# Performance work log

Measured on AMD Instinct MI355X. Metric: run time of the kernel, lower is better.

## Reference

```python
import jax, jax.numpy as jnp
import numpy as np

H = 1024      # embe_size / hidden size
L = 2         # layer_num
LBL = 5       # label_size
B, S = 64, 512


def setup_inputs() -> dict:
    key = jax.random.key(0)
    ks = jax.random.split(key, 7)
    sc = 1.0 / np.sqrt(H)
    inputs = jax.random.normal(ks[0], (B, S, H), dtype=jnp.float32)
    Wx = jax.random.uniform(ks[1], (L, H, 4 * H), minval=-sc, maxval=sc, dtype=jnp.float32)
    bx = jax.random.uniform(ks[2], (L, 4 * H), minval=-sc, maxval=sc, dtype=jnp.float32)
    Wh = jax.random.uniform(ks[3], (L, H, 4 * H), minval=-sc, maxval=sc, dtype=jnp.float32)
    bh = jax.random.uniform(ks[4], (L, 4 * H), minval=-sc, maxval=sc, dtype=jnp.float32)
    scp = 1.0 / np.sqrt(H)
    Wp = jax.random.uniform(ks[5], (H, LBL), minval=-scp, maxval=scp, dtype=jnp.float32)
    bp = jax.random.uniform(ks[6], (LBL,), minval=-scp, maxval=scp, dtype=jnp.float32)
    return {"inputs": inputs, "Wx": Wx, "bx": bx, "Wh": Wh, "bh": bh, "Wp": Wp, "bp": bp}


def _lstm_forward(inputs, Wx, bx, Wh, bh, Wp, bp):
    # inputs: [B,S,H] -> time-major [S,B,H]
    x = jnp.transpose(inputs, (1, 0, 2))
    n_layers = Wx.shape[0]
    bsz, hid = x.shape[1], Wx.shape[1]
    for l in range(n_layers):
        Wh_l, bh_l = Wh[l], bh[l]
        # precompute input->gate projection for all timesteps: [S,B,4H]
        xg = jnp.einsum('sbh,hg->sbg', x, Wx[l]) + bx[l]

        def step(carry, xg_t):
            h, c = carry
            feat = xg_t + h @ Wh_l + bh_l
            i, f, g, o = jnp.split(feat, 4, axis=-1)
            c = jax.nn.sigmoid(f) * c + jax.nn.sigmoid(i) * jnp.tanh(g)
            h = jnp.tanh(c) * jax.nn.sigmoid(o)
            return (h, c), h

        h0 = jnp.zeros((bsz, hid), dtype=x.dtype)
        _, x = jax.lax.scan(step, (h0, h0), xg)
        # dropout is identity at inference (eval mode)
    # max-pool over time (max_pool1d over full seq), then classify
    pooled = jnp.max(x, axis=0)  # [B,H]
    return pooled @ Wp + bp      # [B,label_size]


def reference(inputs, Wx, bx, Wh, bh, Wp, bp):
    return _lstm_forward(inputs, Wx, bx, Wh, bh, Wp, bp)
```

## Files before the change

### kernel.cpp

```cpp
#include <hip/hip_runtime.h>
#include <hip/hip_bf16.h>

typedef _Float16 half8 __attribute__((ext_vector_type(8)));
typedef _Float16 half4v __attribute__((ext_vector_type(4)));
typedef float f32x4 __attribute__((ext_vector_type(4)));

#define BB 64
#define SS 512
#define HH 1024
#define G4 4096
#define NSTEP 514
#define SLOT 65536

#define SB_ARR(g) ((g) * 32)
#define SB_GLB 256
#define SB_GO(g) (288 + (g) * 32)
#define FB_ARR(L, g) ((L) * 256 + (g) * 32)
#define FB_GLB(L) (512 + (L) * 32)
#define FB_GO(L, g) (576 + (L) * 256 + (g) * 32)

__device__ __forceinline__ float sigmf(float x) { return 1.0f / (1.0f + __expf(-x)); }
__device__ __forceinline__ float tanhfast(float x) { return 2.0f / (1.0f + __expf(-2.0f * x)) - 1.0f; }

__device__ __forceinline__ unsigned aload(const unsigned* p) {
  return __hip_atomic_load(p, __ATOMIC_RELAXED, __HIP_MEMORY_SCOPE_AGENT);
}
__device__ __forceinline__ void wait_ge(const unsigned* p, unsigned tgt) {
  while (aload(p) < tgt) __builtin_amdgcn_s_sleep(1);
}
__device__ __forceinline__ unsigned aadd(unsigned* p) {
  return __hip_atomic_fetch_add(p, 1u, __ATOMIC_RELAXED, __HIP_MEMORY_SCOPE_AGENT);
}
__device__ __forceinline__ void astore(unsigned* p, unsigned v) {
  __hip_atomic_store(p, v, __ATOMIC_RELAXED, __HIP_MEMORY_SCOPE_AGENT);
}

__global__ __launch_bounds__(256) void convert_x_kernel(const float* __restrict__ in,
                                                        _Float16* __restrict__ x16) {
  size_t idx = (size_t)blockIdx.x * 256 + threadIdx.x;
  int h4 = (int)(idx & 255);
  int s  = (int)((idx >> 8) & 511);
  int b  = (int)(idx >> 17);
  const float4* src = (const float4*)in;
  float4 v = src[((size_t)b * SS + s) * 256 + h4];
  half4v hv = { (_Float16)v.x, (_Float16)v.y, (_Float16)v.z, (_Float16)v.w };
  *(half4v*)(x16 + ((size_t)s * BB + b) * HH + (size_t)h4 * 4) = hv;
}

__global__ __launch_bounds__(256) void convert_w_kernel(const float* __restrict__ Wx,
                                                        const float* __restrict__ Wh,
                                                        _Float16* __restrict__ wT) {
  __shared__ float tile[32][33];
  int m = blockIdx.x >> 12;
  int t = blockIdx.x & 4095;
  int tn = t & 127, tk = t >> 7;
  int l = m & 1, which = m >> 1;
  const float* src = (which ? Wh : Wx) + (size_t)l * HH * G4;
  int tx = threadIdx.x & 31, ty = threadIdx.x >> 5;
#pragma unroll
  for (int p = 0; p < 4; ++p) {
    int k = tk * 32 + ty + 8 * p, n = tn * 32 + tx;
    tile[ty + 8 * p][tx] = src[(size_t)k * G4 + n];
  }
  __syncthreads();
  _Float16* dst = wT + (size_t)m * G4 * HH;
#pragma unroll
  for (int p = 0; p < 4; ++p) {
    int n = tn * 32 + ty + 8 * p, k = tk * 32 + tx;
    dst[(size_t)n * HH + k] = (_Float16)tile[tx][ty + 8 * p];
  }
}

template <bool TRAJ>
__global__ __launch_bounds__(512, 2) void lstm_persist(
    const _Float16* __restrict__ x16, const _Float16* __restrict__ wT,
    const float* __restrict__ bx, const float* __restrict__ bh,
    _Float16* __restrict__ h1buf, _Float16* __restrict__ h2buf,
    float* __restrict__ hmax, unsigned* __restrict__ bar) {
  __shared__ float part[8][32][72];
  __shared__ float red[64][37];

  const int bid = blockIdx.x;
  const int layer = bid >> 7;
  const int j = bid & 127;
  const int tid = threadIdx.x;
  const int w = tid >> 6, l = tid & 63;
  const int l15 = l & 15, lg = l >> 4;
  const int grp = bid & 7;

  const _Float16* wTe = wT + (size_t)layer * G4 * HH;
  const _Float16* wTr = wT + (size_t)(2 + layer) * G4 * HH;
  const int kbase = w * 128;
  half8 Be[8], Br[8];
#pragma unroll
  for (int kk = 0; kk < 4; ++kk)
#pragma unroll
    for (int c = 0; c < 2; ++c) {
      int nl = 16 * c + l15;
      size_t gcol = (size_t)((nl & 3) * HH + 8 * j + (nl >> 2));
      Be[kk * 2 + c] = *(const half8*)(wTe + gcol * HH + kbase + 32 * kk + 8 * lg);
      Br[kk * 2 + c] = *(const half8*)(wTr + gcol * HH + kbase + 32 * kk + 8 * lg);
    }

  const int erow = tid >> 2, m2 = tid & 3;
  const int hc0 = 8 * j + 2 * m2;
  float bs[8];
  float c0 = 0.f, c1 = 0.f, hm0 = -2.f, hm1 = -2.f;
  if (tid < 256) {
#pragma unroll
    for (int dm = 0; dm < 2; ++dm)
#pragma unroll
      for (int g = 0; g < 4; ++g)
        bs[4 * dm + g] = bx[layer * G4 + g * HH + hc0 + dm] + bh[layer * G4 + g * HH + hc0 + dm];
  }

  const int tmax = TRAJ ? (layer ? NSTEP : SS) : NSTEP;

#pragma unroll 1
  for (int t = 0; t < tmax; ++t) {
    const bool act = (layer == 0) ? (t < SS) : (t >= 2);
    f32x4 acc[8];
#pragma unroll
    for (int i = 0; i < 8; ++i) acc[i] = (f32x4){0.f, 0.f, 0.f, 0.f};

    if (act) {
      const _Float16* Ae;
      if (layer == 0) {
        Ae = x16 + (size_t)t * SLOT;
      } else if (TRAJ) {
        if (tid == 0) wait_ge(bar + FB_GO(0, grp), (unsigned)(t - 1));
        __syncthreads();
        Ae = h1buf + (size_t)(t - 1) * SLOT;
      } else {
        Ae = h1buf + (size_t)((t - 2) & 3) * SLOT;
      }
      const _Float16* aep = Ae + (size_t)l15 * HH + kbase + 8 * lg;
      half8 a[16];
#pragma unroll
      for (int rf = 0; rf < 4; ++rf)
#pragma unroll
        for (int kk = 0; kk < 4; ++kk)
          a[rf * 4 + kk] = *(const half8*)(aep + (size_t)(16 * rf) * HH + 32 * kk);
#pragma unroll
      for (int rf = 0; rf < 4; ++rf)
#pragma unroll
        for (int kk = 0; kk < 4; ++kk) {
          acc[rf * 2 + 0] = __builtin_amdgcn_mfma_f32_16x16x32_f16(a[rf * 4 + kk], Be[kk * 2 + 0], acc[rf * 2 + 0], 0, 0, 0);
          acc[rf * 2 + 1] = __builtin_amdgcn_mfma_f32_16x16x32_f16(a[rf * 4 + kk], Be[kk * 2 + 1], acc[rf * 2 + 1], 0, 0, 0);
        }
    }

    if (tid == 0) {
      if (TRAJ) {
        wait_ge(bar + FB_GO(layer, grp), (unsigned)t);
      } else {
        wait_ge(bar + SB_GO(grp), (unsigned)t);
        __builtin_amdgcn_fence(__ATOMIC_ACQUIRE, "agent");
      }
    }
    __syncthreads();

    if (act) {
      const _Float16* Ah;
      if (layer == 0)
        Ah = TRAJ ? h1buf + (size_t)t * SLOT
                  : h1buf + (size_t)((t - 1) & 3) * SLOT;
      else
        Ah = TRAJ ? h2buf + (size_t)(t - 2) * SLOT
                  : h2buf + (size_t)((t - 1) & 1) * SLOT;
      const _Float16* ahp = Ah + (size_t)l15 * HH + kbase + 8 * lg;
      half8 a[16];
#pragma unroll
      for (int rf = 0; rf < 4; ++rf)
#pragma unroll
        for (int kk = 0; kk < 4; ++kk)
          a[rf * 4 + kk] = *(const half8*)(ahp + (size_t)(16 * rf) * HH + 32 * kk);
#pragma unroll
      for (int rf = 0; rf < 4; ++rf)
#pragma unroll
        for (int kk = 0; kk < 4; ++kk) {
          acc[rf * 2 + 0] = __builtin_amdgcn_mfma_f32_16x16x32_f16(a[rf * 4 + kk], Br[kk * 2 + 0], acc[rf * 2 + 0], 0, 0, 0);
          acc[rf * 2 + 1] = __builtin_amdgcn_mfma_f32_16x16x32_f16(a[rf * 4 + kk], Br[kk * 2 + 1], acc[rf * 2 + 1], 0, 0, 0);
        }

#pragma unroll
      for (int rf = 0; rf < 4; ++rf)
#pragma unroll
        for (int c = 0; c < 2; ++c)
          *(f32x4*)&part[w][16 * c + l15][16 * rf + 4 * lg] = acc[rf * 2 + c];
      __syncthreads();

      {
        int col = tid >> 4, rq = tid & 15;
        f32x4 s = {0.f, 0.f, 0.f, 0.f};
#pragma unroll
        for (int ww = 0; ww < 8; ++ww)
          s += *(const f32x4*)&part[ww][col][4 * rq];
        red[4 * rq + 0][col] = s[0];
        red[4 * rq + 1][col] = s[1];
        red[4 * rq + 2][col] = s[2];
        red[4 * rq + 3][col] = s[3];
      }
      __syncthreads();

      if (tid < 256) {
        float v[8];
#pragma unroll
        for (int q = 0; q < 8; ++q) v[q] = red[erow][8 * m2 + q] + bs[q];
        float i0 = sigmf(v[0]), f0 = sigmf(v[1]), g0 = tanhfast(v[2]), o0 = sigmf(v[3]);
        float i1 = sigmf(v[4]), f1 = sigmf(v[5]), g1 = tanhfast(v[6]), o1 = sigmf(v[7]);
        c0 = f0 * c0 + i0 * g0;
        c1 = f1 * c1 + i1 * g1;
        float h0 = tanhfast(c0) * o0;
        float h1 = tanhfast(c1) * o1;
        if (layer == 1) { hm0 = fmaxf(hm0, h0); hm1 = fmaxf(hm1, h1); }
        _Float16* hout;
        if (layer == 0)
          hout = TRAJ ? h1buf + (size_t)(t + 1) * SLOT : h1buf + (size_t)(t & 3) * SLOT;
        else
          hout = TRAJ ? h2buf + (size_t)(t - 1) * SLOT : h2buf + (size_t)(t & 1) * SLOT;
        unsigned pk = ((unsigned)__builtin_bit_cast(unsigned short, (_Float16)h1) << 16) |
                      (unsigned)__builtin_bit_cast(unsigned short, (_Float16)h0);
        astore((unsigned*)hout + ((erow * HH + hc0) >> 1), pk);
      }
    }

    __syncthreads();
    if (tid == 0) {
      if (TRAJ) {
        unsigned prev = aadd(bar + FB_ARR(layer, grp));
        if (prev == 16u * (unsigned)(t + 1) - 1u) {
          unsigned p2 = aadd(bar + FB_GLB(layer));
          if (p2 == 8u * (unsigned)(t + 1) - 1u) {
#pragma unroll
            for (int gg = 0; gg < 8; ++gg)
              astore(bar + FB_GO(layer, gg), (unsigned)(t + 1));
          }
        }
      } else {
        unsigned prev = aadd(bar + SB_ARR(grp));
        if (prev == 32u * (unsigned)(t + 1) - 1u) {
          unsigned p2 = aadd(bar + SB_GLB);
          if (p2 == 8u * (unsigned)(t + 1) - 1u) {
#pragma unroll
            for (int gg = 0; gg < 8; ++gg)
              astore(bar + SB_GO(gg), (unsigned)(t + 1));
          }
        }
      }
    }
  }

  if (layer == 1 && tid < 256) {
    hmax[erow * HH + hc0]     = hm0;
    hmax[erow * HH + hc0 + 1] = hm1;
  }
}

__global__ __launch_bounds__(320) void classify_kernel(const float* __restrict__ hmax,
                                                       const float* __restrict__ Wp,
                                                       const float* __restrict__ bp,
                                                       float* __restrict__ out) {
  int tid = threadIdx.x;
  int b = tid / 5, jj = tid % 5;
  float s = bp[jj];
  const float* hp = hmax + (size_t)b * HH;
  for (int h = 0; h < HH; ++h) s = fmaf(hp[h], Wp[h * 5 + jj], s);
  out[tid] = s;
}

extern "C" void kernel_launch(void* const* d_in, const int* in_sizes, int n_in,
                              void* d_out, int out_size, void* d_ws, size_t ws_size,
                              hipStream_t stream) {
  const float* inputs = (const float*)d_in[0];
  const float* Wx = (const float*)d_in[1];
  const float* bx = (const float*)d_in[2];
  const float* Wh = (const float*)d_in[3];
  const float* bh = (const float*)d_in[4];
  const float* Wp = (const float*)d_in[5];
  const float* bp = (const float*)d_in[6];
  float* out = (float*)d_out;

  char* ws = (char*)d_ws;
  _Float16* x16 = (_Float16*)(ws + 0);
  _Float16* wT  = (_Float16*)(ws + 67108864);

  const size_t TRAJ_BYTES = (size_t)513 * 131072;
  const size_t NEED_FAST = 100663296ull + 2 * TRAJ_BYTES + 262144 + 8192;
  bool fast = ws_size >= NEED_FAST;

  convert_x_kernel<<<32768, 256, 0, stream>>>(inputs, x16);
  convert_w_kernel<<<16384, 256, 0, stream>>>(Wx, Wh, wT);

  if (fast) {
    _Float16* h1traj = (_Float16*)(ws + 100663296);
    _Float16* h2traj = (_Float16*)(ws + 100663296 + TRAJ_BYTES);
    float* hmax = (float*)(ws + 100663296 + 2 * TRAJ_BYTES);
    unsigned* bar = (unsigned*)(ws + 100663296 + 2 * TRAJ_BYTES + 262144);
    hipMemsetAsync(h1traj, 0, 131072, stream);
    hipMemsetAsync(h2traj, 0, 131072, stream);
    hipMemsetAsync(bar, 0, 8192, stream);
    lstm_persist<true><<<256, 512, 0, stream>>>(x16, wT, bx, bh, h1traj, h2traj, hmax, bar);
    classify_kernel<<<1, 320, 0, stream>>>(hmax, Wp, bp, out);
  } else {
    _Float16* h1buf = (_Float16*)(ws + 100663296);
    _Float16* h2buf = (_Float16*)(ws + 101187584);
    float* hmax = (float*)(ws + 101449728);
    unsigned* bar = (unsigned*)(ws + 101711872);
    hipMemsetAsync(h1buf, 0, 524288, stream);
    hipMemsetAsync(h2buf, 0, 262144, stream);
    hipMemsetAsync(bar, 0, 8192, stream);
    lstm_persist<false><<<256, 512, 0, stream>>>(x16, wT, bx, bh, h1buf, h2buf, hmax, bar);
    classify_kernel<<<1, 320, 0, stream>>>(hmax, Wp, bp, out);
  }
}
```

Measured before the change: 4.822 ms.

## Fuse both LSTM layers into one 128-block persistent kernel with a single barrier

Replaces the 256-block persistent kernel (one layer per block, with separate per-layer barriers) with 128 blocks. Each block computes the same hidden column slice for both layers: waves 0-3 handle layer 0 and waves 4-7 handle layer 1, each over a K range of 256. One grid-wide barrier per step serves both layers, which removes the cross-layer wait and halves the number of barrier participants. In exchange, each wave holds twice as many weight fragments in registers and does twice the MFMA work per step, and only 128 CUs are used. The spin-wait sleep interval is also raised.

```diff
diff --git a/kernel.cpp b/kernel.cpp
--- a/kernel.cpp
+++ b/kernel.cpp
@@ -15,9 +15,9 @@
 #define SB_ARR(g) ((g) * 32)
 #define SB_GLB 256
 #define SB_GO(g) (288 + (g) * 32)
-#define FB_ARR(L, g) ((L) * 256 + (g) * 32)
-#define FB_GLB(L) (512 + (L) * 32)
-#define FB_GO(L, g) (576 + (L) * 256 + (g) * 32)
+#define FU_ARR(g) ((g) * 32)
+#define FU_GLB 256
+#define FU_GO(g) (288 + (g) * 32)
 
 __device__ __forceinline__ float sigmf(float x) { return 1.0f / (1.0f + __expf(-x)); }
 __device__ __forceinline__ float tanhfast(float x) { return 2.0f / (1.0f + __expf(-2.0f * x)) - 1.0f; }
@@ -26,7 +26,7 @@
   return __hip_atomic_load(p, __ATOMIC_RELAXED, __HIP_MEMORY_SCOPE_AGENT);
 }
 __device__ __forceinline__ void wait_ge(const unsigned* p, unsigned tgt) {
-  while (aload(p) < tgt) __builtin_amdgcn_s_sleep(1);
+  while (aload(p) < tgt) __builtin_amdgcn_s_sleep(4);
 }
 __device__ __forceinline__ unsigned aadd(unsigned* p) {
   return __hip_atomic_fetch_add(p, 1u, __ATOMIC_RELAXED, __HIP_MEMORY_SCOPE_AGENT);
@@ -71,8 +71,154 @@
   }
 }
 
-template <bool TRAJ>
-__global__ __launch_bounds__(512, 2) void lstm_persist(
+__global__ __launch_bounds__(512, 2) void lstm_fused(
+    const _Float16* __restrict__ x16, const _Float16* __restrict__ wT,
+    const float* __restrict__ bx, const float* __restrict__ bh,
+    _Float16* __restrict__ h1buf, _Float16* __restrict__ h2buf,
+    float* __restrict__ hmax, unsigned* __restrict__ bar) {
+  __shared__ float part[8][32][72];
+  __shared__ float red[64][68];
+
+  const int bid = blockIdx.x;
+  const int j = bid;
+  const int tid = threadIdx.x;
+  const int w = tid >> 6, l = tid & 63;
+  const int l15 = l & 15, lg = l >> 4;
+  const int grp = bid & 7;
+  const int wlayer = w >> 2;
+  const int kbase = (w & 3) * 256;
+
+  const _Float16* wTe = wT + (size_t)wlayer * G4 * HH;
+  const _Float16* wTr = wT + (size_t)(2 + wlayer) * G4 * HH;
+  half8 Be[16], Br[16];
+#pragma unroll
+  for (int kk = 0; kk < 8; ++kk)
+#pragma unroll
+    for (int c = 0; c < 2; ++c) {
+      int nl = 16 * c + l15;
+      size_t gcol = (size_t)((nl & 3) * HH + 8 * j + (nl >> 2));
+      Be[kk * 2 + c] = *(const half8*)(wTe + gcol * HH + kbase + 32 * kk + 8 * lg);
+      Br[kk * 2 + c] = *(const half8*)(wTr + gcol * HH + kbase + 32 * kk + 8 * lg);
+    }
+
+  const int elayer = tid >> 8;
+  const int erow = (tid & 255) >> 2, m2 = tid & 3;
+  const int hc0 = 8 * j + 2 * m2;
+  float bs[8];
+  float c0 = 0.f, c1 = 0.f, hm0 = -2.f, hm1 = -2.f;
+#pragma unroll
+  for (int dm = 0; dm < 2; ++dm)
+#pragma unroll
+    for (int g = 0; g < 4; ++g)
+      bs[4 * dm + g] = bx[elayer * G4 + g * HH + hc0 + dm] + bh[elayer * G4 + g * HH + hc0 + dm];
+
+#pragma unroll 1
+  for (int t = 0; t < NSTEP; ++t) {
+    const bool wact = wlayer ? (t >= 2) : (t < SS);
+    f32x4 acc[8];
+#pragma unroll
+    for (int i = 0; i < 8; ++i) acc[i] = (f32x4){0.f, 0.f, 0.f, 0.f};
+
+    if (wact) {
+      const _Float16* Ae = (wlayer == 0) ? x16 + (size_t)t * SLOT
+                                         : h1buf + (size_t)(t - 1) * SLOT;
+      const _Float16* aep = Ae + (size_t)l15 * HH + kbase + 8 * lg;
+#pragma unroll
+      for (int rf = 0; rf < 4; ++rf) {
+        half8 av[8];
+#pragma unroll
+        for (int kk = 0; kk < 8; ++kk)
+          av[kk] = *(const half8*)(aep + (size_t)(16 * rf) * HH + 32 * kk);
+#pragma unroll
+        for (int kk = 0; kk < 8; ++kk) {
+          acc[rf * 2 + 0] = __builtin_amdgcn_mfma_f32_16x16x32_f16(av[kk], Be[kk * 2 + 0], acc[rf * 2 + 0], 0, 0, 0);
+          acc[rf * 2 + 1] = __builtin_amdgcn_mfma_f32_16x16x32_f16(av[kk], Be[kk * 2 + 1], acc[rf * 2 + 1], 0, 0, 0);
+        }
+      }
+    }
+
+    if (tid == 0) wait_ge(bar + FU_GO(grp), (unsigned)t);
+    __syncthreads();
+
+    if (wact) {
+      const _Float16* Ah = (wlayer == 0) ? h1buf + (size_t)t * SLOT
+                                         : h2buf + (size_t)(t - 2) * SLOT;
+      const _Float16* ahp = Ah + (size_t)l15 * HH + kbase + 8 * lg;
+#pragma unroll
+      for (int rf = 0; rf < 4; ++rf) {
+        half8 av[8];
+#pragma unroll
+        for (int kk = 0; kk < 8; ++kk)
+          av[kk] = *(const half8*)(ahp + (size_t)(16 * rf) * HH + 32 * kk);
+#pragma unroll
+        for (int kk = 0; kk < 8; ++kk) {
+          acc[rf * 2 + 0] = __builtin_amdgcn_mfma_f32_16x16x32_f16(av[kk], Br[kk * 2 + 0], acc[rf * 2 + 0], 0, 0, 0);
+          acc[rf * 2 + 1] = __builtin_amdgcn_mfma_f32_16x16x32_f16(av[kk], Br[kk * 2 + 1], acc[rf * 2 + 1], 0, 0, 0);
+        }
+      }
+#pragma unroll
+      for (int rf = 0; rf < 4; ++rf)
+#pragma unroll
+        for (int c = 0; c < 2; ++c)
+          *(f32x4*)&part[w][16 * c + l15][16 * rf + 4 * lg] = acc[rf * 2 + c];
+    }
+    __syncthreads();
+
+#pragma unroll
+    for (int sidx = 0; sidx < 2; ++sidx) {
+      int s = tid + 512 * sidx;
+      int L = s >> 9, col = (s >> 4) & 31, rq = s & 15;
+      f32x4 sum = {0.f, 0.f, 0.f, 0.f};
+#pragma unroll
+      for (int ww = 0; ww < 4; ++ww)
+        sum += *(const f32x4*)&part[4 * L + ww][col][4 * rq];
+      red[4 * rq + 0][col + 32 * L] = sum[0];
+      red[4 * rq + 1][col + 32 * L] = sum[1];
+      red[4 * rq + 2][col + 32 * L] = sum[2];
+      red[4 * rq + 3][col + 32 * L] = sum[3];
+    }
+    __syncthreads();
+
+    const bool eact = elayer ? (t >= 2) : (t < SS);
+    if (eact) {
+      float v[8];
+#pragma unroll
+      for (int q = 0; q < 8; ++q) v[q] = red[erow][32 * elayer + 8 * m2 + q] + bs[q];
+      float i0 = sigmf(v[0]), f0 = sigmf(v[1]), g0 = tanhfast(v[2]), o0 = sigmf(v[3]);
+      float i1 = sigmf(v[4]), f1 = sigmf(v[5]), g1 = tanhfast(v[6]), o1 = sigmf(v[7]);
+      c0 = f0 * c0 + i0 * g0;
+      c1 = f1 * c1 + i1 * g1;
+      float h0 = tanhfast(c0) * o0;
+      float h1 = tanhfast(c1) * o1;
+      if (elayer == 1) { hm0 = fmaxf(hm0, h0); hm1 = fmaxf(hm1, h1); }
+      _Float16* hout = (elayer == 0) ? h1buf + (size_t)(t + 1) * SLOT
+                                     : h2buf + (size_t)(t - 1) * SLOT;
+      unsigned pk = ((unsigned)__builtin_bit_cast(unsigned short, (_Float16)h1) << 16) |
+                    (unsigned)__builtin_bit_cast(unsigned short, (_Float16)h0);
+      astore((unsigned*)hout + ((erow * HH + hc0) >> 1), pk);
+    }
+
+    __syncthreads();
+    if (tid == 0) {
+      unsigned prev = aadd(bar + FU_ARR(grp));
+      if (prev == 16u * (unsigned)(t + 1) - 1u) {
+        unsigned p2 = aadd(bar + FU_GLB);
+        if (p2 == 8u * (unsigned)(t + 1) - 1u) {
+#pragma unroll
+          for (int gg = 0; gg < 8; ++gg)
+            astore(bar + FU_GO(gg), (unsigned)(t + 1));
+        }
+      }
+    }
+  }
+
+  if (tid >= 256) {
+    hmax[erow * HH + hc0]     = hm0;
+    hmax[erow * HH + hc0 + 1] = hm1;
+  }
+}
+
+__global__ __launch_bounds__(512, 2) void lstm_safe(
     const _Float16* __restrict__ x16, const _Float16* __restrict__ wT,
     const float* __restrict__ bx, const float* __restrict__ bh,
     _Float16* __restrict__ h1buf, _Float16* __restrict__ h2buf,
@@ -114,26 +260,16 @@
         bs[4 * dm + g] = bx[layer * G4 + g * HH + hc0 + dm] + bh[layer * G4 + g * HH + hc0 + dm];
   }
 
-  const int tmax = TRAJ ? (layer ? NSTEP : SS) : NSTEP;
-
 #pragma unroll 1
-  for (int t = 0; t < tmax; ++t) {
+  for (int t = 0; t < NSTEP; ++t) {
     const bool act = (layer == 0) ? (t < SS) : (t >= 2);
     f32x4 acc[8];
 #pragma unroll
     for (int i = 0; i < 8; ++i) acc[i] = (f32x4){0.f, 0.f, 0.f, 0.f};
 
     if (act) {
-      const _Float16* Ae;
-      if (layer == 0) {
-        Ae = x16 + (size_t)t * SLOT;
-      } else if (TRAJ) {
-        if (tid == 0) wait_ge(bar + FB_GO(0, grp), (unsigned)(t - 1));
-        __syncthreads();
-        Ae = h1buf + (size_t)(t - 1) * SLOT;
-      } else {
-        Ae = h1buf + (size_t)((t - 2) & 3) * SLOT;
-      }
+      const _Float16* Ae = (layer == 0) ? x16 + (size_t)t * SLOT
+                                        : h1buf + (size_t)((t - 2) & 3) * SLOT;
       const _Float16* aep = Ae + (size_t)l15 * HH + kbase + 8 * lg;
       half8 a[16];
 #pragma unroll
@@ -151,23 +287,14 @@
     }
 
     if (tid == 0) {
-      if (TRAJ) {
-        wait_ge(bar + FB_GO(layer, grp), (unsigned)t);
-      } else {
-        wait_ge(bar + SB_GO(grp), (unsigned)t);
-        __builtin_amdgcn_fence(__ATOMIC_ACQUIRE, "agent");
-      }
+      wait_ge(bar + SB_GO(grp), (unsigned)t);
+      __builtin_amdgcn_fence(__ATOMIC_ACQUIRE, "agent");
     }
     __syncthreads();
 
     if (act) {
-      const _Float16* Ah;
-      if (layer == 0)
-        Ah = TRAJ ? h1buf + (size_t)t * SLOT
-                  : h1buf + (size_t)((t - 1) & 3) * SLOT;
-      else
-        Ah = TRAJ ? h2buf + (size_t)(t - 2) * SLOT
-                  : h2buf + (size_t)((t - 1) & 1) * SLOT;
+      const _Float16* Ah = (layer == 0) ? h1buf + (size_t)((t - 1) & 3) * SLOT
+                                        : h2buf + (size_t)((t - 1) & 1) * SLOT;
       const _Float16* ahp = Ah + (size_t)l15 * HH + kbase + 8 * lg;
       half8 a[16];
 #pragma unroll
@@ -214,11 +341,8 @@
         float h0 = tanhfast(c0) * o0;
         float h1 = tanhfast(c1) * o1;
         if (layer == 1) { hm0 = fmaxf(hm0, h0); hm1 = fmaxf(hm1, h1); }
-        _Float16* hout;
-        if (layer == 0)
-          hout = TRAJ ? h1buf + (size_t)(t + 1) * SLOT : h1buf + (size_t)(t & 3) * SLOT;
-        else
-          hout = TRAJ ? h2buf + (size_t)(t - 1) * SLOT : h2buf + (size_t)(t & 1) * SLOT;
+        _Float16* hout = (layer == 0) ? h1buf + (size_t)(t & 3) * SLOT
+                                      : h2buf + (size_t)(t & 1) * SLOT;
         unsigned pk = ((unsigned)__builtin_bit_cast(unsigned short, (_Float16)h1) << 16) |
                       (unsigned)__builtin_bit_cast(unsigned short, (_Float16)h0);
         astore((unsigned*)hout + ((erow * HH + hc0) >> 1), pk);
@@ -227,25 +351,13 @@
 
     __syncthreads();
     if (tid == 0) {
-      if (TRAJ) {
-        unsigned prev = aadd(bar + FB_ARR(layer, grp));
-        if (prev == 16u * (unsigned)(t + 1) - 1u) {
-          unsigned p2 = aadd(bar + FB_GLB(layer));
-          if (p2 == 8u * (unsigned)(t + 1) - 1u) {
-#pragma unroll
-            for (int gg = 0; gg < 8; ++gg)
-              astore(bar + FB_GO(layer, gg), (unsigned)(t + 1));
-          }
-        }
-      } else {
-        unsigned prev = aadd(bar + SB_ARR(grp));
-        if (prev == 32u * (unsigned)(t + 1) - 1u) {
-          unsigned p2 = aadd(bar + SB_GLB);
-          if (p2 == 8u * (unsigned)(t + 1) - 1u) {
-#pragma unroll
-            for (int gg = 0; gg < 8; ++gg)
-              astore(bar + SB_GO(gg), (unsigned)(t + 1));
-          }
+      unsigned prev = aadd(bar + SB_ARR(grp));
+      if (prev == 32u * (unsigned)(t + 1) - 1u) {
+        unsigned p2 = aadd(bar + SB_GLB);
+        if (p2 == 8u * (unsigned)(t + 1) - 1u) {
+#pragma unroll
+          for (int gg = 0; gg < 8; ++gg)
+            astore(bar + SB_GO(gg), (unsigned)(t + 1));
         }
       }
     }
@@ -300,7 +412,7 @@
     hipMemsetAsync(h1traj, 0, 131072, stream);
     hipMemsetAsync(h2traj, 0, 131072, stream);
     hipMemsetAsync(bar, 0, 8192, stream);
-    lstm_persist<true><<<256, 512, 0, stream>>>(x16, wT, bx, bh, h1traj, h2traj, hmax, bar);
+    lstm_fused<<<128, 512, 0, stream>>>(x16, wT, bx, bh, h1traj, h2traj, hmax, bar);
     classify_kernel<<<1, 320, 0, stream>>>(hmax, Wp, bp, out);
   } else {
     _Float16* h1buf = (_Float16*)(ws + 100663296);
@@ -310,7 +422,7 @@
     hipMemsetAsync(h1buf, 0, 524288, stream);
     hipMemsetAsync(h2buf, 0, 262144, stream);
     hipMemsetAsync(bar, 0, 8192, stream);
-    lstm_persist<false><<<256, 512, 0, stream>>>(x16, wT, bx, bh, h1buf, h2buf, hmax, bar);
+    lstm_safe<<<256, 512, 0, stream>>>(x16, wT, bx, bh, h1buf, h2buf, hmax, bar);
     classify_kernel<<<1, 320, 0, stream>>>(hmax, Wp, bp, out);
   }
 }
```

After: 8.714 ms. 80.7% more time.

## Split batch into four 16-row groups and pipeline them through a unified barrier

Applied to the files above, without the earlier changes.

The fast path is replaced by a staggered persistent kernel that processes the batch as four 16-row groups per timestep. Each group gets its own grid-wide barrier phase in a single unified counter scheme shared by both layers, and the next group's input and recurrent operands are prefetched into registers while the current one finishes. Layer 1 now runs one timestep behind layer 0 within the same barrier. The intent is to shorten the serial critical path per barrier and hide load latency. The cost is four times as many barriers per step, each carrying a smaller MFMA workload.

```diff
diff --git a/kernel.cpp b/kernel.cpp
--- a/kernel.cpp
+++ b/kernel.cpp
@@ -9,15 +9,13 @@
 #define SS 512
 #define HH 1024
 #define G4 4096
-#define NSTEP 514
 #define SLOT 65536
 
+#define AR(s) ((s) * 32)
+#define GOW(g) (256 + (g) * 32)
 #define SB_ARR(g) ((g) * 32)
 #define SB_GLB 256
 #define SB_GO(g) (288 + (g) * 32)
-#define FB_ARR(L, g) ((L) * 256 + (g) * 32)
-#define FB_GLB(L) (512 + (L) * 32)
-#define FB_GO(L, g) (576 + (L) * 256 + (g) * 32)
 
 __device__ __forceinline__ float sigmf(float x) { return 1.0f / (1.0f + __expf(-x)); }
 __device__ __forceinline__ float tanhfast(float x) { return 2.0f / (1.0f + __expf(-2.0f * x)) - 1.0f; }
@@ -71,8 +69,161 @@
   }
 }
 
-template <bool TRAJ>
-__global__ __launch_bounds__(512, 2) void lstm_persist(
+#define STEP(G, CA, CR, NA, NR)                                                        \
+  {                                                                                    \
+    const int k = 4 * m + (G);                                                         \
+    if (tid == 0 && k >= 3) wait_ge(bar + GOW(grp), (unsigned)(k - 2));                \
+    __builtin_amdgcn_s_barrier();            \
+    asm volatile("" ::: "memory");                                                     \
+    const bool act = layer ? (m >= 1) : (m < SS);                                      \
+    if (act) {                                                                         \
+      f32x4 acc0 = {0.f, 0.f, 0.f, 0.f};                                               \
+      f32x4 acc1 = {0.f, 0.f, 0.f, 0.f};                                               \
+      _Pragma("unroll") for (int kk = 0; kk < 4; ++kk) {                               \
+        acc0 = __builtin_amdgcn_mfma_f32_16x16x32_f16(CA[kk], Be[kk * 2 + 0], acc0, 0, 0, 0); \
+        acc1 = __builtin_amdgcn_mfma_f32_16x16x32_f16(CA[kk], Be[kk * 2 + 1], acc1, 0, 0, 0); \
+      }                                                                                \
+      _Pragma("unroll") for (int kk = 0; kk < 4; ++kk) {                               \
+        acc0 = __builtin_amdgcn_mfma_f32_16x16x32_f16(CR[kk], Br[kk * 2 + 0], acc0, 0, 0, 0); \
+        acc1 = __builtin_amdgcn_mfma_f32_16x16x32_f16(CR[kk], Br[kk * 2 + 1], acc1, 0, 0, 0); \
+      }                                                                                \
+      *(f32x4*)&part[w][l15][4 * lg] = acc0;                                           \
+      *(f32x4*)&part[w][16 + l15][4 * lg] = acc1;                                      \
+    }                                                                                  \
+    __syncthreads();                                                                   \
+    if (act && tid < 128) {                                                            \
+      int col = tid >> 2, rq = tid & 3;                                                \
+      f32x4 s = {0.f, 0.f, 0.f, 0.f};                                                  \
+      _Pragma("unroll") for (int ww = 0; ww < 8; ++ww)                                 \
+          s += *(const f32x4*)&part[ww][col][4 * rq];                                  \
+      red[4 * rq + 0][col] = s[0];                                                     \
+      red[4 * rq + 1][col] = s[1];                                                     \
+      red[4 * rq + 2][col] = s[2];                                                     \
+      red[4 * rq + 3][col] = s[3];                                                     \
+    }                                                                                  \
+    __syncthreads();                                                                   \
+    if (act && tid < 64) {                                                             \
+      float v[8];                                                                      \
+      _Pragma("unroll") for (int q = 0; q < 8; ++q) v[q] = red[er][8 * m2 + q] + bs[q];\
+      float i0 = sigmf(v[0]), f0 = sigmf(v[1]), g0 = tanhfast(v[2]), o0 = sigmf(v[3]); \
+      float i1 = sigmf(v[4]), f1 = sigmf(v[5]), g1 = tanhfast(v[6]), o1 = sigmf(v[7]); \
+      float cn0 = f0 * cs0[(G)] + i0 * g0;                                             \
+      float cn1 = f1 * cs1[(G)] + i1 * g1;                                             \
+      cs0[(G)] = cn0; cs1[(G)] = cn1;                                                  \
+      float h0 = tanhfast(cn0) * o0;                                                   \
+      float h1 = tanhfast(cn1) * o1;                                                   \
+      if (layer == 1) { hx0[(G)] = fmaxf(hx0[(G)], h0); hx1[(G)] = fmaxf(hx1[(G)], h1); } \
+      _Float16* hout = (layer == 0) ? h1buf + (size_t)(m + 1) * SLOT                   \
+                                    : h2buf + (size_t)m * SLOT;                        \
+      int row = 16 * (G) + er;                                                         \
+      unsigned pk = ((unsigned)__builtin_bit_cast(unsigned short, (_Float16)h1) << 16) | \
+                    (unsigned)__builtin_bit_cast(unsigned short, (_Float16)h0);        \
+      astore((unsigned*)hout + ((row * HH + hc0) >> 1), pk);                           \
+    }                                                                                  \
+    __syncthreads();                \
+    if (tid == 0) {                                                                    \
+      unsigned prev = aadd(bar + AR(k & 7));                                           \
+      if (prev == 256u * (unsigned)(k >> 3) + 255u) {                                  \
+        _Pragma("unroll") for (int gg = 0; gg < 8; ++gg)                               \
+            astore(bar + GOW(gg), (unsigned)(k + 1));                                  \
+      }                                                                                \
+    }                                                                                  \
+    {  \
+      const int gn = ((G) + 1) & 3;                                                    \
+      const int mn = ((G) == 3) ? m + 1 : m;                                           \
+      if (layer == 0) {                                                                \
+        if (mn < SS) {                                                                 \
+          const _Float16* pa = x16 + (size_t)mn * SLOT + (size_t)(16 * gn + l15) * HH + kbase + 8 * lg;   \
+          const _Float16* pr = h1buf + (size_t)mn * SLOT + (size_t)(16 * gn + l15) * HH + kbase + 8 * lg; \
+          _Pragma("unroll") for (int kk = 0; kk < 4; ++kk) {                           \
+            NA[kk] = *(const half8*)(pa + 32 * kk);                                    \
+            NR[kk] = *(const half8*)(pr + 32 * kk);                                    \
+          }                                                                            \
+        }                                                                              \
+      } else {                                                                         \
+        if (mn >= 1 && mn <= SS) {                                                     \
+          const _Float16* pa = h1buf + (size_t)mn * SLOT + (size_t)(16 * gn + l15) * HH + kbase + 8 * lg;       \
+          const _Float16* pr = h2buf + (size_t)(mn - 1) * SLOT + (size_t)(16 * gn + l15) * HH + kbase + 8 * lg; \
+          _Pragma("unroll") for (int kk = 0; kk < 4; ++kk) {                           \
+            NA[kk] = *(const half8*)(pa + 32 * kk);                                    \
+            NR[kk] = *(const half8*)(pr + 32 * kk);                                    \
+          }                                                                            \
+        }                                                                              \
+      }                                                                                \
+    }                                                                                  \
+  }
+
+__global__ __launch_bounds__(512, 2) void lstm_stagger(
+    const _Float16* __restrict__ x16, const _Float16* __restrict__ wT,
+    const float* __restrict__ bx, const float* __restrict__ bh,
+    _Float16* __restrict__ h1buf, _Float16* __restrict__ h2buf,
+    float* __restrict__ hmax, unsigned* __restrict__ bar) {
+  __shared__ float part[8][32][20];
+  __shared__ float red[16][36];
+
+  const int bid = blockIdx.x;
+  const int layer = bid >> 7;
+  const int j = bid & 127;
+  const int grp = bid & 7;
+  const int tid = threadIdx.x;
+  const int w = tid >> 6, l = tid & 63;
+  const int l15 = l & 15, lg = l >> 4;
+
+  const _Float16* wTe = wT + (size_t)layer * G4 * HH;
+  const _Float16* wTr = wT + (size_t)(2 + layer) * G4 * HH;
+  const int kbase = w * 128;
+  half8 Be[8], Br[8];
+#pragma unroll
+  for (int kk = 0; kk < 4; ++kk)
+#pragma unroll
+    for (int c = 0; c < 2; ++c) {
+      int nl = 16 * c + l15;
+      size_t gcol = (size_t)((nl & 3) * HH + 8 * j + (nl >> 2));
+      Be[kk * 2 + c] = *(const half8*)(wTe + gcol * HH + kbase + 32 * kk + 8 * lg);
+      Br[kk * 2 + c] = *(const half8*)(wTr + gcol * HH + kbase + 32 * kk + 8 * lg);
+    }
+
+  const int er = tid >> 2, m2 = tid & 3;
+  const int hc0 = 8 * j + 2 * m2;
+  float bs[8];
+#pragma unroll
+  for (int dm = 0; dm < 2; ++dm)
+#pragma unroll
+    for (int g = 0; g < 4; ++g)
+      bs[4 * dm + g] = bx[layer * G4 + g * HH + hc0 + dm] + bh[layer * G4 + g * HH + hc0 + dm];
+  float cs0[4] = {0.f, 0.f, 0.f, 0.f}, cs1[4] = {0.f, 0.f, 0.f, 0.f};
+  float hx0[4] = {-2.f, -2.f, -2.f, -2.f}, hx1[4] = {-2.f, -2.f, -2.f, -2.f};
+
+  half8 p0A[4], p0R[4], p1A[4], p1R[4];
+  if (layer == 0) {
+    const _Float16* pa = x16 + (size_t)l15 * HH + kbase + 8 * lg;
+    const _Float16* pr = h1buf + (size_t)l15 * HH + kbase + 8 * lg;
+#pragma unroll
+    for (int kk = 0; kk < 4; ++kk) {
+      p0A[kk] = *(const half8*)(pa + 32 * kk);
+      p0R[kk] = *(const half8*)(pr + 32 * kk);
+    }
+  }
+
+#pragma unroll 1
+  for (int m = 0; m <= SS; ++m) {
+    STEP(0, p0A, p0R, p1A, p1R)
+    STEP(1, p1A, p1R, p0A, p0R)
+    STEP(2, p0A, p0R, p1A, p1R)
+    STEP(3, p1A, p1R, p0A, p0R)
+  }
+
+  if (layer == 1 && tid < 64) {
+#pragma unroll
+    for (int g = 0; g < 4; ++g) {
+      int row = 16 * g + er;
+      hmax[row * HH + hc0]     = hx0[g];
+      hmax[row * HH + hc0 + 1] = hx1[g];
+    }
+  }
+}
+
+__global__ __launch_bounds__(512, 2) void lstm_safe(
     const _Float16* __restrict__ x16, const _Float16* __restrict__ wT,
     const float* __restrict__ bx, const float* __restrict__ bh,
     _Float16* __restrict__ h1buf, _Float16* __restrict__ h2buf,
@@ -114,26 +265,16 @@
         bs[4 * dm + g] = bx[layer * G4 + g * HH + hc0 + dm] + bh[layer * G4 + g * HH + hc0 + dm];
   }
 
-  const int tmax = TRAJ ? (layer ? NSTEP : SS) : NSTEP;
-
 #pragma unroll 1
-  for (int t = 0; t < tmax; ++t) {
+  for (int t = 0; t < SS + 2; ++t) {
     const bool act = (layer == 0) ? (t < SS) : (t >= 2);
     f32x4 acc[8];
 #pragma unroll
     for (int i = 0; i < 8; ++i) acc[i] = (f32x4){0.f, 0.f, 0.f, 0.f};
 
     if (act) {
-      const _Float16* Ae;
-      if (layer == 0) {
-        Ae = x16 + (size_t)t * SLOT;
-      } else if (TRAJ) {
-        if (tid == 0) wait_ge(bar + FB_GO(0, grp), (unsigned)(t - 1));
-        __syncthreads();
-        Ae = h1buf + (size_t)(t - 1) * SLOT;
-      } else {
-        Ae = h1buf + (size_t)((t - 2) & 3) * SLOT;
-      }
+      const _Float16* Ae = (layer == 0) ? x16 + (size_t)t * SLOT
+                                        : h1buf + (size_t)((t - 2) & 3) * SLOT;
       const _Float16* aep = Ae + (size_t)l15 * HH + kbase + 8 * lg;
       half8 a[16];
 #pragma unroll
@@ -151,23 +292,14 @@
     }
 
     if (tid == 0) {
-      if (TRAJ) {
-        wait_ge(bar + FB_GO(layer, grp), (unsigned)t);
-      } else {
-        wait_ge(bar + SB_GO(grp), (unsigned)t);
-        __builtin_amdgcn_fence(__ATOMIC_ACQUIRE, "agent");
-      }
+      wait_ge(bar + SB_GO(grp), (unsigned)t);
+      __builtin_amdgcn_fence(__ATOMIC_ACQUIRE, "agent");
     }
     __syncthreads();
 
     if (act) {
-      const _Float16* Ah;
-      if (layer == 0)
-        Ah = TRAJ ? h1buf + (size_t)t * SLOT
-                  : h1buf + (size_t)((t - 1) & 3) * SLOT;
-      else
-        Ah = TRAJ ? h2buf + (size_t)(t - 2) * SLOT
-                  : h2buf + (size_t)((t - 1) & 1) * SLOT;
+      const _Float16* Ah = (layer == 0) ? h1buf + (size_t)((t - 1) & 3) * SLOT
+                                        : h2buf + (size_t)((t - 1) & 1) * SLOT;
       const _Float16* ahp = Ah + (size_t)l15 * HH + kbase + 8 * lg;
       half8 a[16];
 #pragma unroll
@@ -214,11 +346,8 @@
         float h0 = tanhfast(c0) * o0;
         float h1 = tanhfast(c1) * o1;
         if (layer == 1) { hm0 = fmaxf(hm0, h0); hm1 = fmaxf(hm1, h1); }
-        _Float16* hout;
-        if (layer == 0)
-          hout = TRAJ ? h1buf + (size_t)(t + 1) * SLOT : h1buf + (size_t)(t & 3) * SLOT;
-        else
-          hout = TRAJ ? h2buf + (size_t)(t - 1) * SLOT : h2buf + (size_t)(t & 1) * SLOT;
+        _Float16* hout = (layer == 0) ? h1buf + (size_t)(t & 3) * SLOT
+                                      : h2buf + (size_t)(t & 1) * SLOT;
         unsigned pk = ((unsigned)__builtin_bit_cast(unsigned short, (_Float16)h1) << 16) |
                       (unsigned)__builtin_bit_cast(unsigned short, (_Float16)h0);
         astore((unsigned*)hout + ((erow * HH + hc0) >> 1), pk);
@@ -227,25 +356,13 @@
 
     __syncthreads();
     if (tid == 0) {
-      if (TRAJ) {
-        unsigned prev = aadd(bar + FB_ARR(layer, grp));
-        if (prev == 16u * (unsigned)(t + 1) - 1u) {
-          unsigned p2 = aadd(bar + FB_GLB(layer));
-          if (p2 == 8u * (unsigned)(t + 1) - 1u) {
-#pragma unroll
-            for (int gg = 0; gg < 8; ++gg)
-              astore(bar + FB_GO(layer, gg), (unsigned)(t + 1));
-          }
-        }
-      } else {
-        unsigned prev = aadd(bar + SB_ARR(grp));
-        if (prev == 32u * (unsigned)(t + 1) - 1u) {
-          unsigned p2 = aadd(bar + SB_GLB);
-          if (p2 == 8u * (unsigned)(t + 1) - 1u) {
-#pragma unroll
-            for (int gg = 0; gg < 8; ++gg)
-              astore(bar + SB_GO(gg), (unsigned)(t + 1));
-          }
+      unsigned prev = aadd(bar + SB_ARR(grp));
+      if (prev == 32u * (unsigned)(t + 1) - 1u) {
+        unsigned p2 = aadd(bar + SB_GLB);
+        if (p2 == 8u * (unsigned)(t + 1) - 1u) {
+#pragma unroll
+          for (int gg = 0; gg < 8; ++gg)
+            astore(bar + SB_GO(gg), (unsigned)(t + 1));
         }
       }
     }
@@ -300,7 +417,7 @@
     hipMemsetAsync(h1traj, 0, 131072, stream);
     hipMemsetAsync(h2traj, 0, 131072, stream);
     hipMemsetAsync(bar, 0, 8192, stream);
-    lstm_persist<true><<<256, 512, 0, stream>>>(x16, wT, bx, bh, h1traj, h2traj, hmax, bar);
+    lstm_stagger<<<256, 512, 0, stream>>>(x16, wT, bx, bh, h1traj, h2traj, hmax, bar);
     classify_kernel<<<1, 320, 0, stream>>>(hmax, Wp, bp, out);
   } else {
     _Float16* h1buf = (_Float16*)(ws + 100663296);
@@ -310,7 +427,7 @@
     hipMemsetAsync(h1buf, 0, 524288, stream);
     hipMemsetAsync(h2buf, 0, 262144, stream);
     hipMemsetAsync(bar, 0, 8192, stream);
-    lstm_persist<false><<<256, 512, 0, stream>>>(x16, wT, bx, bh, h1buf, h2buf, hmax, bar);
+    lstm_safe<<<256, 512, 0, stream>>>(x16, wT, bx, bh, h1buf, h2buf, hmax, bar);
     classify_kernel<<<1, 320, 0, stream>>>(hmax, Wp, bp, out);
   }
 }
```

After: 6.233 ms. +29.3%, slower.
